# Kernel optimization log

Hardware: AMD Instinct MI355X
Metric: run time of the kernel (lower is better)

The kernel has to match this reference:

```python
import jax, jax.numpy as jnp
import numpy as np

HIDDEN = 1024
SEQ = 32768


def setup_inputs() -> dict:
    key = jax.random.key(0)
    k1, k2, k3, k4 = jax.random.split(key, 4)
    scale = 1.0 / np.sqrt(HIDDEN)
    return {
        "hidden": jax.random.normal(k1, (HIDDEN,), dtype=jnp.float32),
        "encoder_outputs": jax.random.normal(k2, (SEQ, HIDDEN), dtype=jnp.float32),
        "W": jax.random.normal(k3, (HIDDEN, HIDDEN), dtype=jnp.float32) * scale,
        "b": jax.random.normal(k4, (HIDDEN,), dtype=jnp.float32) * scale,
    }


def reference(hidden, encoder_outputs, W, b):
    # method == 'general': energy_i = Linear(enc_i); score_i = hidden . energy_i
    # Batched: energies = (enc @ W.T + b) @ hidden   -> [S]
    proj = jnp.einsum("sh,oh->so", encoder_outputs, W) + b  # [S, H]
    energies = proj @ hidden                                  # [S]
    attn = jax.nn.softmax(energies, axis=-1)                  # softmax over seq
    return attn[None, None, :]                                # [1, 1, S]
```

## Files before the change

### kernel.cpp

```cpp
#include <hip/hip_runtime.h>
#include <math.h>

#define H 1024
#define S 32768

__global__ void matvec_partial_kernel(const float* __restrict__ W,
                                      const float* __restrict__ hidden,
                                      float* __restrict__ vpart) {
    const int t = threadIdx.x;
    const int b = blockIdx.x;
    const int h4 = t * 4;
    const int o0 = b * 4;
    float4 acc = make_float4(0.f, 0.f, 0.f, 0.f);
#pragma unroll
    for (int i = 0; i < 4; ++i) {
        const float  hv = hidden[o0 + i];
        const float4 w  = *reinterpret_cast<const float4*>(&W[(size_t)(o0 + i) * H + h4]);
        acc.x += hv * w.x; acc.y += hv * w.y;
        acc.z += hv * w.z; acc.w += hv * w.w;
    }
    *reinterpret_cast<float4*>(&vpart[(size_t)b * H + h4]) = acc;
}

__global__ void matvec_reduce_kernel(const float* __restrict__ vpart,
                                     float* __restrict__ v) {
    const int idx = blockIdx.x * 64 + threadIdx.x;
    const int h4 = idx * 4;
    float4 acc = make_float4(0.f, 0.f, 0.f, 0.f);
#pragma unroll 8
    for (int p = 0; p < 256; ++p) {
        const float4 q = *reinterpret_cast<const float4*>(&vpart[(size_t)p * H + h4]);
        acc.x += q.x; acc.y += q.y; acc.z += q.z; acc.w += q.w;
    }
    *reinterpret_cast<float4*>(&v[h4]) = acc;
}

__global__ void energies_kernel(const float* __restrict__ enc,
                                const float* __restrict__ v,
                                float* __restrict__ energies,
                                float* __restrict__ mpart,
                                float* __restrict__ spart) {
    const int wave = threadIdx.x >> 6;
    const int lane = threadIdx.x & 63;
    const int gwave = blockIdx.x * 4 + wave;
    const int s0 = gwave * 4;

    float4 vv[4];
#pragma unroll
    for (int j = 0; j < 4; ++j)
        vv[j] = *reinterpret_cast<const float4*>(&v[j * 256 + lane * 4]);

    float e[4];
#pragma unroll
    for (int r = 0; r < 4; ++r) {
        const float* row = enc + (size_t)(s0 + r) * H;
        float acc = 0.f;
#pragma unroll
        for (int j = 0; j < 4; ++j) {
            const float4 ev = *reinterpret_cast<const float4*>(&row[j * 256 + lane * 4]);
            acc += ev.x * vv[j].x + ev.y * vv[j].y + ev.z * vv[j].z + ev.w * vv[j].w;
        }
#pragma unroll
        for (int off = 32; off > 0; off >>= 1)
            acc += __shfl_xor(acc, off, 64);
        e[r] = acc;
    }

    if (lane == 0) {
        energies[s0 + 0] = e[0];
        energies[s0 + 1] = e[1];
        energies[s0 + 2] = e[2];
        energies[s0 + 3] = e[3];
    }

    const float mw = fmaxf(fmaxf(e[0], e[1]), fmaxf(e[2], e[3]));
    const float sw = __expf(e[0] - mw) + __expf(e[1] - mw) +
                     __expf(e[2] - mw) + __expf(e[3] - mw);

    __shared__ float lm[4], ls[4];
    if (lane == 0) { lm[wave] = mw; ls[wave] = sw; }
    __syncthreads();
    if (threadIdx.x == 0) {
        const float m = fmaxf(fmaxf(lm[0], lm[1]), fmaxf(lm[2], lm[3]));
        const float s = ls[0] * __expf(lm[0] - m) + ls[1] * __expf(lm[1] - m) +
                        ls[2] * __expf(lm[2] - m) + ls[3] * __expf(lm[3] - m);
        mpart[blockIdx.x] = m;
        spart[blockIdx.x] = s;
    }
}

__global__ void finalize_kernel(const float* __restrict__ energies,
                                const float* __restrict__ mpart,
                                const float* __restrict__ spart,
                                float* __restrict__ out) {
    const int t = threadIdx.x;
    const int lane = t & 63;
    const int wave = t >> 6;
    __shared__ float rm[4], rs[4];

    const float4 ma = *reinterpret_cast<const float4*>(&mpart[t * 8]);
    const float4 mb = *reinterpret_cast<const float4*>(&mpart[t * 8 + 4]);
    const float4 sa = *reinterpret_cast<const float4*>(&spart[t * 8]);
    const float4 sb = *reinterpret_cast<const float4*>(&spart[t * 8 + 4]);

    float mt = fmaxf(fmaxf(fmaxf(ma.x, ma.y), fmaxf(ma.z, ma.w)),
                     fmaxf(fmaxf(mb.x, mb.y), fmaxf(mb.z, mb.w)));
#pragma unroll
    for (int off = 32; off > 0; off >>= 1)
        mt = fmaxf(mt, __shfl_xor(mt, off, 64));
    if (lane == 0) rm[wave] = mt;
    __syncthreads();
    const float gm = fmaxf(fmaxf(rm[0], rm[1]), fmaxf(rm[2], rm[3]));

    float st = sa.x * __expf(ma.x - gm) + sa.y * __expf(ma.y - gm) +
               sa.z * __expf(ma.z - gm) + sa.w * __expf(ma.w - gm) +
               sb.x * __expf(mb.x - gm) + sb.y * __expf(mb.y - gm) +
               sb.z * __expf(mb.z - gm) + sb.w * __expf(mb.w - gm);
#pragma unroll
    for (int off = 32; off > 0; off >>= 1)
        st += __shfl_xor(st, off, 64);
    if (lane == 0) rs[wave] = st;
    __syncthreads();
    const float inv = 1.0f / (rs[0] + rs[1] + rs[2] + rs[3]);

    const int i = blockIdx.x * 256 + t;
    out[i] = __expf(energies[i] - gm) * inv;
}

extern "C" void kernel_launch(void* const* d_in, const int* in_sizes, int n_in,
                              void* d_out, int out_size, void* d_ws, size_t ws_size,
                              hipStream_t stream) {
    const float* hidden = (const float*)d_in[0];
    const float* enc    = (const float*)d_in[1];
    const float* W      = (const float*)d_in[2];
    float* out = (float*)d_out;

    float* vpart    = (float*)d_ws;
    float* v        = vpart + 256 * H;
    float* energies = v + H;
    float* mpart    = energies + S;
    float* spart    = mpart + 2048;

    matvec_partial_kernel<<<256, 256, 0, stream>>>(W, hidden, vpart);
    matvec_reduce_kernel<<<4, 64, 0, stream>>>(vpart, v);
    energies_kernel<<<2048, 256, 0, stream>>>(enc, v, energies, mpart, spart);
    finalize_kernel<<<128, 256, 0, stream>>>(energies, mpart, spart, out);
}
```

Before: 218.5 us.

## Fuse W^T·hidden matvec into one kernel and batch encoder row loads

```diff
diff --git a/kernel.cpp b/kernel.cpp
--- a/kernel.cpp
+++ b/kernel.cpp
@@ -4,35 +4,43 @@
 #define H 1024
 #define S 32768
 
-__global__ void matvec_partial_kernel(const float* __restrict__ W,
-                                      const float* __restrict__ hidden,
-                                      float* __restrict__ vpart) {
+__global__ void matvec_v_kernel(const float* __restrict__ W,
+                                const float* __restrict__ hidden,
+                                float* __restrict__ v) {
+    __shared__ float sh[H];
+    __shared__ float4 red[256];
     const int t = threadIdx.x;
     const int b = blockIdx.x;
-    const int h4 = t * 4;
-    const int o0 = b * 4;
+    const int c = t & 7;
+    const int j = t >> 3;
+
+    *reinterpret_cast<float4*>(&sh[t * 4]) =
+        *reinterpret_cast<const float4*>(&hidden[t * 4]);
+    __syncthreads();
+
+    const int colbase = b * 32 + c * 4;
     float4 acc = make_float4(0.f, 0.f, 0.f, 0.f);
-#pragma unroll
-    for (int i = 0; i < 4; ++i) {
-        const float  hv = hidden[o0 + i];
-        const float4 w  = *reinterpret_cast<const float4*>(&W[(size_t)(o0 + i) * H + h4]);
+#pragma unroll 8
+    for (int k = 0; k < 32; ++k) {
+        const int o = j + 32 * k;
+        const float hv = sh[o];
+        const float4 w = *reinterpret_cast<const float4*>(&W[(size_t)o * H + colbase]);
         acc.x += hv * w.x; acc.y += hv * w.y;
         acc.z += hv * w.z; acc.w += hv * w.w;
     }
-    *reinterpret_cast<float4*>(&vpart[(size_t)b * H + h4]) = acc;
-}
-
-__global__ void matvec_reduce_kernel(const float* __restrict__ vpart,
-                                     float* __restrict__ v) {
-    const int idx = blockIdx.x * 64 + threadIdx.x;
-    const int h4 = idx * 4;
-    float4 acc = make_float4(0.f, 0.f, 0.f, 0.f);
-#pragma unroll 8
-    for (int p = 0; p < 256; ++p) {
-        const float4 q = *reinterpret_cast<const float4*>(&vpart[(size_t)p * H + h4]);
-        acc.x += q.x; acc.y += q.y; acc.z += q.z; acc.w += q.w;
+    red[t] = acc;
+    __syncthreads();
+#pragma unroll
+    for (int off = 128; off >= 8; off >>= 1) {
+        if (t < off) {
+            float4 a = red[t], bb = red[t + off];
+            a.x += bb.x; a.y += bb.y; a.z += bb.z; a.w += bb.w;
+            red[t] = a;
+        }
+        __syncthreads();
     }
-    *reinterpret_cast<float4*>(&v[h4]) = acc;
+    if (t < 8)
+        *reinterpret_cast<float4*>(&v[b * 32 + t * 4]) = red[t];
 }
 
 __global__ void energies_kernel(const float* __restrict__ enc,
@@ -50,15 +58,24 @@
     for (int j = 0; j < 4; ++j)
         vv[j] = *reinterpret_cast<const float4*>(&v[j * 256 + lane * 4]);
 
+    float4 ev[4][4];
+#pragma unroll
+    for (int r = 0; r < 4; ++r) {
+        const float* row = enc + (size_t)(s0 + r) * H;
+#pragma unroll
+        for (int j = 0; j < 4; ++j)
+            ev[r][j] = *reinterpret_cast<const float4*>(&row[j * 256 + lane * 4]);
+    }
+
     float e[4];
 #pragma unroll
     for (int r = 0; r < 4; ++r) {
-        const float* row = enc + (size_t)(s0 + r) * H;
-        float acc = 0.f;
+        float acc = ev[r][0].x * vv[0].x + ev[r][0].y * vv[0].y +
+                    ev[r][0].z * vv[0].z + ev[r][0].w * vv[0].w;
 #pragma unroll
-        for (int j = 0; j < 4; ++j) {
-            const float4 ev = *reinterpret_cast<const float4*>(&row[j * 256 + lane * 4]);
-            acc += ev.x * vv[j].x + ev.y * vv[j].y + ev.z * vv[j].z + ev.w * vv[j].w;
+        for (int j = 1; j < 4; ++j) {
+            acc += ev[r][j].x * vv[j].x + ev[r][j].y * vv[j].y +
+                   ev[r][j].z * vv[j].z + ev[r][j].w * vv[j].w;
         }
 #pragma unroll
         for (int off = 32; off > 0; off >>= 1)
@@ -135,14 +152,12 @@
     const float* W      = (const float*)d_in[2];
     float* out = (float*)d_out;
 
-    float* vpart    = (float*)d_ws;
-    float* v        = vpart + 256 * H;
+    float* v        = (float*)d_ws;
     float* energies = v + H;
     float* mpart    = energies + S;
     float* spart    = mpart + 2048;
 
-    matvec_partial_kernel<<<256, 256, 0, stream>>>(W, hidden, vpart);
-    matvec_reduce_kernel<<<4, 64, 0, stream>>>(vpart, v);
+    matvec_v_kernel<<<32, 256, 0, stream>>>(W, hidden, v);
     energies_kernel<<<2048, 256, 0, stream>>>(enc, v, energies, mpart, spart);
     finalize_kernel<<<128, 256, 0, stream>>>(energies, mpart, spart, out);
 }
```

New measurement: 206.6 us. -5.4%, faster.
